# Kernel tuning notes

Hardware: AMD Instinct MI355X
Metric: run time of the kernel (lower is better)

The kernel has to match this reference:

```python
import jax, jax.numpy as jnp
import numpy as np

IMG_W, IMG_H = 1242.0, 375.0
NEG = jnp.float32(-10.0)

def _make_boxes(key, n, max_w, max_h):
    k1, k2, k3, k4 = jax.random.split(key, 4)
    x1 = jax.random.uniform(k1, (n,), minval=0.0, maxval=IMG_W - 8.0)
    y1 = jax.random.uniform(k2, (n,), minval=0.0, maxval=IMG_H - 8.0)
    w = jax.random.uniform(k3, (n,), minval=4.0, maxval=max_w)
    h = jax.random.uniform(k4, (n,), minval=4.0, maxval=max_h)
    x2 = jnp.minimum(x1 + w, IMG_W)
    y2 = jnp.minimum(y1 + h, IMG_H)
    return jnp.stack([x1, y1, x2, y2], axis=-1).astype(jnp.float32)

def setup_inputs() -> dict:
    key = jax.random.key(0)
    kb, kq, k3, k2, kd = jax.random.split(key, 5)
    N, K = 10000, 500
    boxes = _make_boxes(kb, N, 300.0, 150.0)        # projected 3D boxes [N,4]
    query_boxes = _make_boxes(kq, K, 300.0, 150.0)  # 2D detections  [K,4]
    scores_3d = jax.random.uniform(k3, (N, 1), dtype=jnp.float32)
    scores_2d = jax.random.uniform(k2, (K, 1), dtype=jnp.float32)
    dis_to_lidar_3d = jax.random.uniform(kd, (N, 1), dtype=jnp.float32) * 82.0 / 82.0
    return {"boxes": boxes, "query_boxes": query_boxes, "scores_3d": scores_3d,
            "scores_2d": scores_2d, "dis_to_lidar_3d": dis_to_lidar_3d, "criterion": -1}

def reference(boxes, query_boxes, scores_3d, scores_2d, dis_to_lidar_3d, criterion):
    K = query_boxes.shape[0]
    N = boxes.shape[0]
    bx1, by1, bx2, by2 = boxes[:, 0], boxes[:, 1], boxes[:, 2], boxes[:, 3]   # [N]
    qx1, qy1, qx2, qy2 = (query_boxes[:, 0], query_boxes[:, 1],
                          query_boxes[:, 2], query_boxes[:, 3])               # [K]
    # pairwise intersection widths/heights [K, N]
    iw = jnp.minimum(bx2[None, :], qx2[:, None]) - jnp.maximum(bx1[None, :], qx1[:, None])
    ih = jnp.minimum(by2[None, :], qy2[:, None]) - jnp.maximum(by1[None, :], qy1[:, None])
    valid = (iw > 0) & (ih > 0)
    inter = iw * ih
    box_area = (bx2 - bx1) * (by2 - by1)    # [N]
    qbox_area = (qx2 - qx1) * (qy2 - qy1)   # [K]
    if criterion == -1:
        ua = box_area[None, :] + qbox_area[:, None] - inter
    elif criterion == 0:
        ua = jnp.broadcast_to(box_area[None, :], (K, N))
    elif criterion == 1:
        ua = jnp.broadcast_to(qbox_area[:, None], (K, N))
    else:
        ua = jnp.ones((K, N), dtype=boxes.dtype)
    iou = inter / ua
    # Dense association tensor [K, N, 4]: valid pairs carry (iou, s3d, s2d, dis);
    # invalid pairs carry the (-10, s3d, -10, dis) sentinel pattern the numba
    # kernel writes for unmatched 3D boxes.
    c0 = jnp.where(valid, iou, NEG)
    c1 = jnp.broadcast_to(scores_3d[None, :, 0], (K, N))
    c2 = jnp.where(valid, scores_2d[:, 0:1], NEG)
    c3 = jnp.broadcast_to(dis_to_lidar_3d[None, :, 0], (K, N))
    overlaps = jnp.stack([c0, c1, c2, c3], axis=-1).reshape(K * N, 4)
    kk, nn = jnp.meshgrid(jnp.arange(K, dtype=jnp.int32),
                          jnp.arange(N, dtype=jnp.int32), indexing="ij")
    tensor_index = jnp.stack([kk, nn], axis=-1).reshape(K * N, 2)
    return overlaps, tensor_index, valid.reshape(K * N)
```

## Files before the change

kernel.cpp:

```cpp
#include <hip/hip_runtime.h>
#include <stdint.h>

typedef float float4v __attribute__((ext_vector_type(4)));
typedef float float2v __attribute__((ext_vector_type(2)));

__device__ __forceinline__ int read_crit(const void* p) {
    const int ci = *(const int*)p;
    if (ci >= -2 && ci <= 3) return ci;
    const float cf = *(const float*)p;
    if (cf == cf && fabsf(cf) <= 4.0f && cf == truncf(cf)) return (int)cf;
    return -1;
}

#define KPB 10

__global__ __launch_bounds__(256) void clocs_kernel(
    const float4v* __restrict__ boxes,
    const float4v* __restrict__ qboxes,
    const float*   __restrict__ s3d,
    const float*   __restrict__ s2d,
    const float*   __restrict__ dis,
    const void*    __restrict__ crit_p,
    float*         __restrict__ out,
    int N, int K)
{
    const int n = blockIdx.x * blockDim.x + threadIdx.x;
    if (n >= N) return;
    const int k0 = blockIdx.y * KPB;

    const int crit = read_crit(crit_p);

    const float4v b  = boxes[n];
    const float   s3 = s3d[n];
    const float   dl = dis[n];
    const float barea = (b.z - b.x) * (b.w - b.y);
    const float nf = (float)n;

    const size_t KN = (size_t)K * (size_t)N;

    #pragma unroll
    for (int kk = 0; kk < KPB; ++kk) {
        const int k = k0 + kk;

        const float4v qb = qboxes[k];
        const float qarea = (qb.z - qb.x) * (qb.w - qb.y);
        const float sc2   = s2d[k];

        const float iw = fminf(b.z, qb.z) - fmaxf(b.x, qb.x);
        const float ih = fminf(b.w, qb.w) - fmaxf(b.y, qb.y);
        const bool  valid = (iw > 0.0f) && (ih > 0.0f);
        const float inter = iw * ih;
        float ua;
        if (crit == -1)      ua = barea + qarea - inter;
        else if (crit == 0)  ua = barea;
        else if (crit == 1)  ua = qarea;
        else                 ua = 1.0f;
        const float iou = (ua != 0.0f) ? (inter / ua) : 0.0f;

        float4v ov;
        ov.x = valid ? iou : -10.0f;
        ov.y = s3;
        ov.z = valid ? sc2 : -10.0f;
        ov.w = dl;

        float2v ix;
        ix.x = (float)k;
        ix.y = nf;

        const size_t p = (size_t)k * (size_t)N + (size_t)n;

        *(float4v*)(out + p * 4)          = ov;
        *(float2v*)(out + KN * 4 + p * 2) = ix;
        *(out + KN * 6 + p)               = valid ? 1.0f : 0.0f;
    }
}

extern "C" void kernel_launch(void* const* d_in, const int* in_sizes, int n_in,
                              void* d_out, int out_size, void* d_ws, size_t ws_size,
                              hipStream_t stream) {
    const float4v* boxes  = (const float4v*)d_in[0];
    const float4v* qboxes = (const float4v*)d_in[1];
    const float*   s3d    = (const float*)d_in[2];
    const float*   s2d    = (const float*)d_in[3];
    const float*   dis    = (const float*)d_in[4];

    const int N = in_sizes[0] / 4;
    const int K = in_sizes[1] / 4;
    const int block = 256;
    dim3 grid((N + block - 1) / block, K / KPB, 1);

    clocs_kernel<<<grid, dim3(block, 1, 1), 0, stream>>>(
        boxes, qboxes, s3d, s2d, dis, d_in[5],
        (float*)d_out, N, K);
}
```

Measured before the change: 27.68 us.

## Split output regions across grid z-slices with wider per-thread stores

The kernel now handles one query box per block row. It uses a third grid dimension to write the three output regions separately: the overlaps tensor, the index pairs, and the valid mask. The index and valid writers each cover two columns per thread, so they issue 16-byte and 8-byte stores instead of 8-byte and 4-byte ones. The aim is to make each block's write stream contiguous within a single region, which should improve store coalescing in this write-bound kernel. In exchange, the valid test is computed twice, the grid is much larger, about half the index and valid blocks exit immediately, and an odd N would make those paths read and write past the end of their region.

```diff
diff --git a/kernel.cpp b/kernel.cpp
--- a/kernel.cpp
+++ b/kernel.cpp
@@ -3,6 +3,8 @@
 
 typedef float float4v __attribute__((ext_vector_type(4)));
 typedef float float2v __attribute__((ext_vector_type(2)));
+
+#define BLK 256
 
 __device__ __forceinline__ int read_crit(const void* p) {
     const int ci = *(const int*)p;
@@ -11,8 +13,6 @@
     if (cf == cf && fabsf(cf) <= 4.0f && cf == truncf(cf)) return (int)cf;
     return -1;
 }
-
-#define KPB 10
 
 __global__ __launch_bounds__(256) void clocs_kernel(
     const float4v* __restrict__ boxes,
@@ -24,32 +24,28 @@
     float*         __restrict__ out,
     int N, int K)
 {
-    const int n = blockIdx.x * blockDim.x + threadIdx.x;
-    if (n >= N) return;
-    const int k0 = blockIdx.y * KPB;
-
-    const int crit = read_crit(crit_p);
-
-    const float4v b  = boxes[n];
-    const float   s3 = s3d[n];
-    const float   dl = dis[n];
-    const float barea = (b.z - b.x) * (b.w - b.y);
-    const float nf = (float)n;
-
+    const int k = blockIdx.y;
+    const int z = blockIdx.z;
     const size_t KN = (size_t)K * (size_t)N;
 
-    #pragma unroll
-    for (int kk = 0; kk < KPB; ++kk) {
-        const int k = k0 + kk;
+    if (z == 0) {
+        const int n = blockIdx.x * BLK + threadIdx.x;
+        if (n >= N) return;
 
         const float4v qb = qboxes[k];
         const float qarea = (qb.z - qb.x) * (qb.w - qb.y);
         const float sc2   = s2d[k];
+        const int   crit  = read_crit(crit_p);
+
+        const float4v b  = boxes[n];
+        const float   s3 = s3d[n];
+        const float   dl = dis[n];
 
         const float iw = fminf(b.z, qb.z) - fmaxf(b.x, qb.x);
         const float ih = fminf(b.w, qb.w) - fmaxf(b.y, qb.y);
         const bool  valid = (iw > 0.0f) && (ih > 0.0f);
         const float inter = iw * ih;
+        const float barea = (b.z - b.x) * (b.w - b.y);
         float ua;
         if (crit == -1)      ua = barea + qarea - inter;
         else if (crit == 0)  ua = barea;
@@ -63,15 +59,42 @@
         ov.z = valid ? sc2 : -10.0f;
         ov.w = dl;
 
-        float2v ix;
-        ix.x = (float)k;
-        ix.y = nf;
+        const size_t p = (size_t)k * (size_t)N + (size_t)n;
+        *(float4v*)(out + p * 4) = ov;
+
+    } else if (z == 1) {
+        const int n = (blockIdx.x * BLK + threadIdx.x) * 2;
+        if (n >= N) return;
+
+        float4v ix;
+        ix.x = (float)k; ix.y = (float)n;
+        ix.z = (float)k; ix.w = (float)(n + 1);
 
         const size_t p = (size_t)k * (size_t)N + (size_t)n;
+        *(float4v*)(out + KN * 4 + p * 2) = ix;
 
-        *(float4v*)(out + p * 4)          = ov;
-        *(float2v*)(out + KN * 4 + p * 2) = ix;
-        *(out + KN * 6 + p)               = valid ? 1.0f : 0.0f;
+    } else {
+        const int n = (blockIdx.x * BLK + threadIdx.x) * 2;
+        if (n >= N) return;
+
+        const float4v qb = qboxes[k];
+        const float4v b0 = boxes[n + 0];
+        const float4v b1 = boxes[n + 1];
+
+        float2v v;
+        {
+            const float iw = fminf(b0.z, qb.z) - fmaxf(b0.x, qb.x);
+            const float ih = fminf(b0.w, qb.w) - fmaxf(b0.y, qb.y);
+            v.x = (iw > 0.0f && ih > 0.0f) ? 1.0f : 0.0f;
+        }
+        {
+            const float iw = fminf(b1.z, qb.z) - fmaxf(b1.x, qb.x);
+            const float ih = fminf(b1.w, qb.w) - fmaxf(b1.y, qb.y);
+            v.y = (iw > 0.0f && ih > 0.0f) ? 1.0f : 0.0f;
+        }
+
+        const size_t p = (size_t)k * (size_t)N + (size_t)n;
+        *(float2v*)(out + KN * 6 + p) = v;
     }
 }
 
@@ -86,10 +109,9 @@
 
     const int N = in_sizes[0] / 4;
     const int K = in_sizes[1] / 4;
-    const int block = 256;
-    dim3 grid((N + block - 1) / block, K / KPB, 1);
+    dim3 grid((N + BLK - 1) / BLK, K, 3);
 
-    clocs_kernel<<<grid, dim3(block, 1, 1), 0, stream>>>(
+    clocs_kernel<<<grid, dim3(BLK, 1, 1), 0, stream>>>(
         boxes, qboxes, s3d, s2d, dis, d_in[5],
         (float*)d_out, N, K);
 }
```

Result: slower. 30.35 us (+9.6%).
